# Optimization experiments

Measured on AMD Instinct MI355X. Metric: run time of the kernel, lower is better.

Reference implementation:

```python
import jax, jax.numpy as jnp
import numpy as np

OMEGA_ENC = 0.01   # Encoder.omega
OMEGA_K = 0.1      # KernelMLP.omega
N0, E0 = 4096, 16384     # level-0 graph
N1, E1 = 1024, 8192      # level-1 (pooled) graph
F_IN, H, LAT, DIM = 8, 64, 32, 3
F = H + DIM              # conv input features (x || pos)


def _glorot(key, shape):
    s = jnp.sqrt(2.0 / (shape[0] + shape[-1]))
    return (jax.random.normal(key, shape) * s).astype(jnp.float32)


def setup_inputs() -> dict:
    key = jax.random.key(0)
    ks = jax.random.split(key, 24)
    inp = {
        "x": jax.random.normal(ks[0], (N0, F_IN), jnp.float32),
        "pos": jax.random.normal(ks[1], (N0, DIM), jnp.float32),
        "edge_index": jax.random.randint(ks[2], (2, E0), 0, N0),
        "pool_edge_index1": jax.random.randint(ks[3], (2, E1), 0, N1),
        "pool_pos1": jax.random.normal(ks[4], (N1, DIM), jnp.float32),
        "pool_keep_idx0": jnp.sort(jax.random.randint(ks[5], (N1,), 0, N0)),
        "lin0_w": _glorot(ks[6], (F_IN, H)),
        "lin0_b": 0.01 * jax.random.normal(ks[7], (H,), jnp.float32),
        "lin1_w": _glorot(ks[8], (H, LAT)),
        "lin1_b": 0.01 * jax.random.normal(ks[9], (LAT,), jnp.float32),
    }
    k = 10
    for i in range(2):
        inp[f"conv{i}_k_w0"] = _glorot(ks[k], (DIM + 1, H))
        inp[f"conv{i}_k_b0"] = 0.01 * jax.random.normal(ks[k + 1], (H,), jnp.float32)
        inp[f"conv{i}_k_w1"] = _glorot(ks[k + 2], (H, H))
        inp[f"conv{i}_k_b1"] = 0.01 * jax.random.normal(ks[k + 3], (H,), jnp.float32)
        inp[f"conv{i}_k_w2"] = _glorot(ks[k + 4], (H, F))
        inp[f"conv{i}_k_b2"] = 0.01 * jax.random.normal(ks[k + 5], (F,), jnp.float32)
        inp[f"conv{i}_bias"] = jnp.zeros((H,), jnp.float32)  # zeros() init in torch
        k += 6
    return inp


def _with_self_loops(ei, n):
    # add_remaining_self_loops: input edges are assumed self-loop-free
    loops = jnp.arange(n, dtype=ei.dtype)
    return jnp.concatenate([ei, jnp.stack([loops, loops])], axis=1)


def _kernel_conv(xf, ei, pos, n, w0, b0, w1, b1, w2, b2, bias):
    src, dst = ei[0], ei[1]
    rel = pos[dst] - pos[src]                               # [E,3]
    zero = jnp.all(rel == 0.0, axis=1)                      # self loops -> rho=0, nan phi in torch
    rel_s = jnp.where(zero[:, None], 1.0, rel)              # safe values (avoid nan grads)
    rho = jnp.sqrt(jnp.sum(rel_s * rel_s, axis=1))
    theta = jnp.arctan2(rel_s[:, 1], rel_s[:, 0])
    phi = jnp.arcsin(jnp.clip(rel_s[:, 2] / rho, -1.0, 1.0))
    # torch sets theta/phi to 0 where phi is nan (rho==0); rho itself is 0 there
    rho = jnp.where(zero, 0.0, rho)
    theta = jnp.where(zero, 0.0, theta)
    phi = jnp.where(zero, 0.0, phi)
    feats = jnp.stack([rho, theta / jnp.pi, phi / jnp.pi], axis=1)   # [E,3]
    # KernelMLP lin0 on (feats || channel_id), evaluated for all out channels at once
    base = feats @ w0[:DIM] + b0                            # [E,H]
    ch = jnp.arange(H, dtype=xf.dtype)                      # out_channels == H
    h0 = jnp.sin(OMEGA_K * (base[None] + ch[:, None, None] * w0[DIM][None, None]))  # [C,E,H]
    h1 = jnp.sin(OMEGA_K * (jnp.einsum('ceh,hk->cek', h0, w1) + b1))                # [C,E,H]
    x_j = xf[src]                                           # [E,F]
    # msg[e,c] = (lin2(h1[c,e]) * x_j[e]).sum(); lin2 folded into the contraction
    msg = jnp.einsum('ceh,hf,ef->ec', h1, w2, x_j) + (x_j @ b2)[:, None]            # [E,C]
    return jax.ops.segment_sum(msg, dst, num_segments=n) + bias


def reference(x, edge_index, pos, pool_edge_index1, pool_pos1, pool_keep_idx0,
              lin0_w, lin0_b, lin1_w, lin1_b,
              conv0_k_w0, conv0_k_b0, conv0_k_w1, conv0_k_b1, conv0_k_w2, conv0_k_b2, conv0_bias,
              conv1_k_w0, conv1_k_b0, conv1_k_w1, conv1_k_b1, conv1_k_w2, conv1_k_b2, conv1_bias):
    n0 = x.shape[0]
    h = jnp.sin(OMEGA_ENC * (x @ lin0_w + lin0_b))
    ei0 = _with_self_loops(edge_index, n0)
    h = jnp.sin(OMEGA_ENC * _kernel_conv(jnp.concatenate([h, pos], 1), ei0, pos, n0,
                                         conv0_k_w0, conv0_k_b0, conv0_k_w1, conv0_k_b1,
                                         conv0_k_w2, conv0_k_b2, conv0_bias))
    # max_pool_neighbor_x: per-node max over neighbors incl. self (self loops in ei0)
    h = jax.ops.segment_max(h[ei0[0]], ei0[1], num_segments=n0)[pool_keep_idx0]
    n1 = pool_pos1.shape[0]
    ei1 = _with_self_loops(pool_edge_index1, n1)
    h = jnp.sin(OMEGA_ENC * _kernel_conv(jnp.concatenate([h, pool_pos1], 1), ei1, pool_pos1, n1,
                                         conv1_k_w0, conv1_k_b0, conv1_k_w1, conv1_k_b1,
                                         conv1_k_w2, conv1_k_b2, conv1_bias))
    return jnp.sin(OMEGA_ENC * (h @ lin1_w + lin1_b))   # [N1, LAT]
```

## Files before the change

kernel.cpp:

```cpp
#include <hip/hip_runtime.h>
#include <hip/hip_fp16.h>

#define N0C 4096
#define E0C 16384
#define N1C 1024
#define E1C 8192
#define HC 64
#define FINC 8
#define LATC 32
#define FC 67
#define E0T (E0C + N0C)
#define E1T (E1C + N1C)

typedef float f32x4 __attribute__((ext_vector_type(4)));
typedef _Float16 f16x8 __attribute__((ext_vector_type(8)));

__global__ void k_misc(const float* __restrict__ c0w0, const float* __restrict__ c1w0,
                       const float* __restrict__ c0w1, const float* __restrict__ c1w1,
                       const float* __restrict__ c0w2, const float* __restrict__ c1w2,
                       const int* __restrict__ ei0, const int* __restrict__ ei1,
                       _Float16* __restrict__ bC0, _Float16* __restrict__ bS0,
                       _Float16* __restrict__ bC1, _Float16* __restrict__ bS1,
                       _Float16* __restrict__ w1f0, _Float16* __restrict__ w1f1,
                       float* __restrict__ w2t0, float* __restrict__ w2t1,
                       int* __restrict__ cnt) {
  int id = blockIdx.x * blockDim.x + threadIdx.x;
  if (id < 8192) {
    int lvl = id >> 12, r = id & 4095;
    int fi = r >> 9, lane = (r >> 3) & 63, j = r & 7;
    int nt = fi & 3, ks = fi >> 2;
    int c = nt * 16 + (lane & 15);
    int h = ks * 32 + (lane >> 4) * 8 + j;
    const float* w = lvl ? c1w0 : c0w0;
    float s, cv;
    sincosf(0.1f * (float)c * w[3 * HC + h], &s, &cv);
    (lvl ? bC1 : bC0)[r] = (_Float16)cv;
    (lvl ? bS1 : bS0)[r] = (_Float16)s;
  } else if (id < 16384) {
    int r0 = id - 8192;
    int lvl = r0 >> 12, r = r0 & 4095;
    int fi = r >> 9, lane = (r >> 3) & 63, j = r & 7;
    int ms = fi & 3, ks = fi >> 2;
    int h = ks * 32 + (lane >> 4) * 8 + j;
    int kout = ms * 16 + (lane & 15);
    const float* w = lvl ? c1w1 : c0w1;
    (lvl ? w1f1 : w1f0)[r] = (_Float16)w[h * HC + kout];
  } else if (id < 24960) {
    int r = id - 16384;
    int lvl = r >= FC * HC;
    r -= lvl * FC * HC;
    int f = r >> 6, k = r & 63;
    (lvl ? w2t1 : w2t0)[r] = (lvl ? c1w2 : c0w2)[k * FC + f];
  } else if (id < 54656) {
    int r = id - 24960;
    if (r < E0T) {
      int dst = (r < E0C) ? ei0[E0C + r] : (r - E0C);
      atomicAdd(cnt + dst, 1);
    } else {
      int e = r - E0T;
      int dst = (e < E1C) ? ei1[E1C + e] : (e - E1C);
      atomicAdd(cnt + N0C + dst, 1);
    }
  }
}

__global__ void k_scan(const int* __restrict__ cnt, int* __restrict__ rp0,
                       int* __restrict__ rp1) {
  __shared__ int s[1024];
  const int b = blockIdx.x;
  const int n = b ? N1C : N0C;
  const int* c = cnt + (b ? N0C : 0);
  int* rp = b ? rp1 : rp0;
  const int tid = threadIdx.x;
  const int per = n >> 10;
  int loc[4];
  int sum = 0;
  for (int j = 0; j < per; ++j) { loc[j] = c[tid * per + j]; sum += loc[j]; }
  s[tid] = sum;
  __syncthreads();
  for (int off = 1; off < 1024; off <<= 1) {
    int v = s[tid] + ((tid >= off) ? s[tid - off] : 0);
    __syncthreads();
    s[tid] = v;
    __syncthreads();
  }
  int base = tid ? s[tid - 1] : 0;
  for (int j = 0; j < per; ++j) { rp[tid * per + j] = base; base += loc[j]; }
  if (tid == 1023) rp[n] = s[1023];
}

__global__ void k_scatter(const int* __restrict__ ei0, const int* __restrict__ ei1,
                          const int* __restrict__ rp0, const int* __restrict__ rp1,
                          int* __restrict__ fill, int* __restrict__ eidx0,
                          int* __restrict__ eidx1) {
  int id = blockIdx.x * blockDim.x + threadIdx.x;
  if (id < E0T) {
    int dst = (id < E0C) ? ei0[E0C + id] : (id - E0C);
    eidx0[rp0[dst] + atomicAdd(fill + dst, 1)] = id;
  } else if (id < E0T + E1T) {
    int e = id - E0T;
    int dst = (e < E1C) ? ei1[E1C + e] : (e - E1C);
    eidx1[rp1[dst] + atomicAdd(fill + N0C + dst, 1)] = e;
  }
}

__global__ void k_node0(const float* __restrict__ x, const float* __restrict__ l0w,
                        const float* __restrict__ l0b, const float* __restrict__ posp,
                        const float* __restrict__ w2t, const float* __restrict__ b2,
                        float* __restrict__ tN, float* __restrict__ dN) {
  __shared__ float xr[4][64];
  const int wave = threadIdx.x >> 6, lane = threadIdx.x & 63;
  const int n = blockIdx.x * 4 + wave;
  float a = l0b[lane];
#pragma unroll
  for (int f = 0; f < FINC; ++f) a = fmaf(x[n * FINC + f], l0w[f * HC + lane], a);
  xr[wave][lane] = sinf(0.01f * a);
  __syncthreads();
  const float px = posp[n * 3], py = posp[n * 3 + 1], pz = posp[n * 3 + 2];
  float tl = 0.f, ds = 0.f;
#pragma unroll 8
  for (int f = 0; f < HC; ++f) {
    float xv = xr[wave][f];
    tl = fmaf(xv, w2t[f * HC + lane], tl);
    ds = fmaf(xv, b2[f], ds);
  }
  tl = fmaf(px, w2t[64 * HC + lane], fmaf(py, w2t[65 * HC + lane], fmaf(pz, w2t[66 * HC + lane], tl)));
  ds = fmaf(px, b2[64], fmaf(py, b2[65], fmaf(pz, b2[66], ds)));
  tN[n * HC + lane] = tl;
  if (lane == 0) dN[n] = ds;
}

__global__ __launch_bounds__(256, 2) void k_conv(
    const int* __restrict__ ei, int E, int eTot,
    const float* __restrict__ posp,
    const float* __restrict__ tN, const float* __restrict__ dN,
    const float* __restrict__ kw0, const float* __restrict__ kb0,
    const _Float16* __restrict__ bC, const _Float16* __restrict__ bS,
    const _Float16* __restrict__ w1f, const float* __restrict__ b1,
    float* __restrict__ msg) {
  __shared__ _Float16 scS[4][64], scC[4][64];
  const int tid = threadIdx.x;
  const int wave = tid >> 6, lane = tid & 63;
  const int q = lane >> 4;

  f16x8 w1r[8], cbr[8], sbr[8];
#pragma unroll
  for (int f = 0; f < 8; ++f) {
    w1r[f] = *(const f16x8*)(w1f + ((f << 6) + lane) * 8);
    cbr[f] = *(const f16x8*)(bC + ((f << 6) + lane) * 8);
    sbr[f] = *(const f16x8*)(bS + ((f << 6) + lane) * 8);
  }
  const float kb0v = kb0[lane];
  const float kw0x = kw0[lane], kw0y = kw0[HC + lane], kw0z = kw0[2 * HC + lane];

  const int nW = gridDim.x * 4;
  for (int e = blockIdx.x * 4 + wave; e < eTot; e += nW) {
    int s, d2;
    if (e < E) { s = ei[e]; d2 = ei[E + e]; } else { s = e - E; d2 = s; }
    const float px = posp[s * 3], py = posp[s * 3 + 1], pz = posp[s * 3 + 2];
    const float rx = posp[d2 * 3] - px;
    const float ry = posp[d2 * 3 + 1] - py;
    const float rz = posp[d2 * 3 + 2] - pz;
    float f0 = 0.f, f1 = 0.f, f2 = 0.f;
    if (!(rx == 0.f && ry == 0.f && rz == 0.f)) {
      const float PI_F = 3.14159265358979323846f;
      float rho = sqrtf(rx * rx + ry * ry + rz * rz);
      float th = atan2f(ry, rx);
      float ratio = fminf(1.f, fmaxf(-1.f, rz / rho));
      float ph = asinf(ratio);
      f0 = rho; f1 = th / PI_F; f2 = ph / PI_F;
    }
    float base = fmaf(f0, kw0x, fmaf(f1, kw0y, fmaf(f2, kw0z, kb0v)));
    float sv, cv;
    sincosf(0.1f * base, &sv, &cv);
    scS[wave][lane] = (_Float16)sv;
    scC[wave][lane] = (_Float16)cv;
    __builtin_amdgcn_wave_barrier();

    f16x8 bf[2][4];
#pragma unroll
    for (int ks = 0; ks < 2; ++ks) {
      f16x8 sv8 = *(const f16x8*)&scS[wave][ks * 32 + q * 8];
      f16x8 cv8 = *(const f16x8*)&scC[wave][ks * 32 + q * 8];
#pragma unroll
      for (int nt = 0; nt < 4; ++nt)
        bf[ks][nt] = sv8 * cbr[ks * 4 + nt] + cv8 * sbr[ks * 4 + nt];
    }

    f32x4 acc[4][4];
    const f32x4 zero = {0.f, 0.f, 0.f, 0.f};
#pragma unroll
    for (int ms = 0; ms < 4; ++ms)
#pragma unroll
      for (int nt = 0; nt < 4; ++nt) acc[ms][nt] = zero;
#pragma unroll
    for (int ks = 0; ks < 2; ++ks)
#pragma unroll
      for (int ms = 0; ms < 4; ++ms)
#pragma unroll
        for (int nt = 0; nt < 4; ++nt)
          acc[ms][nt] = __builtin_amdgcn_mfma_f32_16x16x32_f16(
              w1r[ks * 4 + ms], bf[ks][nt], acc[ms][nt], 0, 0, 0);

    const float dv = dN[s];
    float snt0 = 0.f, snt1 = 0.f, snt2 = 0.f, snt3 = 0.f;
#pragma unroll
    for (int ms = 0; ms < 4; ++ms) {
      f32x4 tv = *(const f32x4*)(tN + (size_t)s * HC + ms * 16 + q * 4);
      f32x4 bv = *(const f32x4*)(b1 + ms * 16 + q * 4);
#pragma unroll
      for (int r = 0; r < 4; ++r) {
        float bb = 0.1f * bv[r], tt = tv[r];
        snt0 = fmaf(__sinf(fmaf(0.1f, acc[ms][0][r], bb)), tt, snt0);
        snt1 = fmaf(__sinf(fmaf(0.1f, acc[ms][1][r], bb)), tt, snt1);
        snt2 = fmaf(__sinf(fmaf(0.1f, acc[ms][2][r], bb)), tt, snt2);
        snt3 = fmaf(__sinf(fmaf(0.1f, acc[ms][3][r], bb)), tt, snt3);
      }
    }
    snt0 += __shfl_xor(snt0, 16, 64); snt0 += __shfl_xor(snt0, 32, 64);
    snt1 += __shfl_xor(snt1, 16, 64); snt1 += __shfl_xor(snt1, 32, 64);
    snt2 += __shfl_xor(snt2, 16, 64); snt2 += __shfl_xor(snt2, 32, 64);
    snt3 += __shfl_xor(snt3, 16, 64); snt3 += __shfl_xor(snt3, 32, 64);
    float val = (q == 0) ? snt0 : (q == 1) ? snt1 : (q == 2) ? snt2 : snt3;
    msg[(size_t)e * HC + lane] = val + dv;
  }
}

__global__ void k_reduce(const float* __restrict__ msg, const int* __restrict__ eidx,
                         const int* __restrict__ rp, const float* __restrict__ bias,
                         float* __restrict__ outp, int n) {
  int wave = threadIdx.x >> 6, lane = threadIdx.x & 63;
  int node = blockIdx.x * 4 + wave;
  if (node >= n) return;
  int j0 = rp[node], j1 = rp[node + 1];
  float s = 0.f;
  for (int j = j0; j < j1; ++j) s += msg[(size_t)eidx[j] * HC + lane];
  outp[node * HC + lane] = sinf(0.01f * (s + bias[lane]));
}

__global__ void k_pool1(const float* __restrict__ hc0, const int* __restrict__ eidx,
                        const int* __restrict__ rp, const int* __restrict__ ei,
                        const int* __restrict__ keep, const float* __restrict__ ppos,
                        const float* __restrict__ w2t, const float* __restrict__ b2,
                        float* __restrict__ tN, float* __restrict__ dN) {
  __shared__ float xr[4][64];
  const int wave = threadIdx.x >> 6, lane = threadIdx.x & 63;
  const int i = blockIdx.x * 4 + wave;
  int n = keep[i];
  int j0 = rp[n], j1 = rp[n + 1];
  float m = -INFINITY;
  for (int j = j0; j < j1; ++j) {
    int e = eidx[j];
    int src = (e < E0C) ? ei[e] : (e - E0C);
    m = fmaxf(m, hc0[(size_t)src * HC + lane]);
  }
  xr[wave][lane] = m;
  __syncthreads();
  const float px = ppos[i * 3], py = ppos[i * 3 + 1], pz = ppos[i * 3 + 2];
  float tl = 0.f, ds = 0.f;
#pragma unroll 8
  for (int f = 0; f < HC; ++f) {
    float xv = xr[wave][f];
    tl = fmaf(xv, w2t[f * HC + lane], tl);
    ds = fmaf(xv, b2[f], ds);
  }
  tl = fmaf(px, w2t[64 * HC + lane], fmaf(py, w2t[65 * HC + lane], fmaf(pz, w2t[66 * HC + lane], tl)));
  ds = fmaf(px, b2[64], fmaf(py, b2[65], fmaf(pz, b2[66], ds)));
  tN[i * HC + lane] = tl;
  if (lane == 0) dN[i] = ds;
}

__global__ void k_reduce1f(const float* __restrict__ msg, const int* __restrict__ eidx,
                           const int* __restrict__ rp, const float* __restrict__ bias,
                           const float* __restrict__ l1w, const float* __restrict__ l1b,
                           float* __restrict__ outp) {
  __shared__ float hr[4][64];
  const int wave = threadIdx.x >> 6, lane = threadIdx.x & 63;
  const int node = blockIdx.x * 4 + wave;
  int j0 = rp[node], j1 = rp[node + 1];
  float s = 0.f;
  for (int j = j0; j < j1; ++j) s += msg[(size_t)eidx[j] * HC + lane];
  hr[wave][lane] = sinf(0.01f * (s + bias[lane]));
  __syncthreads();
  if (lane < 32) {
    float o = l1b[lane];
#pragma unroll 8
    for (int c = 0; c < HC; ++c) o = fmaf(hr[wave][c], l1w[c * LATC + lane], o);
    outp[node * LATC + lane] = sinf(0.01f * o);
  }
}

extern "C" void kernel_launch(void* const* d_in, const int* in_sizes, int n_in,
                              void* d_out, int out_size, void* d_ws, size_t ws_size,
                              hipStream_t stream) {
  (void)in_sizes; (void)n_in; (void)out_size; (void)ws_size;
  const float* x    = (const float*)d_in[0];
  const float* pos  = (const float*)d_in[1];
  const int*   ei   = (const int*)d_in[2];
  const int*   pei  = (const int*)d_in[3];
  const float* ppos = (const float*)d_in[4];
  const int*   keep = (const int*)d_in[5];
  const float* l0w  = (const float*)d_in[6];
  const float* l0b  = (const float*)d_in[7];
  const float* l1w  = (const float*)d_in[8];
  const float* l1b  = (const float*)d_in[9];
  const float* c0w0 = (const float*)d_in[10];
  const float* c0b0 = (const float*)d_in[11];
  const float* c0w1 = (const float*)d_in[12];
  const float* c0b1 = (const float*)d_in[13];
  const float* c0w2 = (const float*)d_in[14];
  const float* c0b2 = (const float*)d_in[15];
  const float* c0bias = (const float*)d_in[16];
  const float* c1w0 = (const float*)d_in[17];
  const float* c1b0 = (const float*)d_in[18];
  const float* c1w1 = (const float*)d_in[19];
  const float* c1b1 = (const float*)d_in[20];
  const float* c1w2 = (const float*)d_in[21];
  const float* c1b2 = (const float*)d_in[22];
  const float* c1bias = (const float*)d_in[23];
  float* outp = (float*)d_out;

  char* p = (char*)d_ws;
  auto carve = [&](size_t bytes) -> char* {
    char* r = p;
    p += (bytes + 255) & ~(size_t)255;
    return r;
  };
  float* hc0  = (float*)carve((size_t)N0C * HC * 4);
  float* tN0  = (float*)carve((size_t)N0C * HC * 4);
  float* dN0  = (float*)carve((size_t)N0C * 4);
  float* tN1  = (float*)carve((size_t)N1C * HC * 4);
  float* dN1  = (float*)carve((size_t)N1C * 4);
  _Float16* bC0  = (_Float16*)carve(4096 * 2);
  _Float16* bS0  = (_Float16*)carve(4096 * 2);
  _Float16* bC1  = (_Float16*)carve(4096 * 2);
  _Float16* bS1  = (_Float16*)carve(4096 * 2);
  _Float16* w1f0 = (_Float16*)carve(4096 * 2);
  _Float16* w1f1 = (_Float16*)carve(4096 * 2);
  float* w2t0 = (float*)carve((size_t)FC * HC * 4);
  float* w2t1 = (float*)carve((size_t)FC * HC * 4);
  int* cnt  = (int*)carve((size_t)(N0C + N1C) * 4);
  int* fill = (int*)carve((size_t)(N0C + N1C) * 4);
  int* rp0 = (int*)carve((size_t)(N0C + 1) * 4);
  int* rp1 = (int*)carve((size_t)(N1C + 1) * 4);
  int* eidx0 = (int*)carve((size_t)E0T * 4);
  int* eidx1 = (int*)carve((size_t)E1T * 4);
  float* msg = (float*)carve((size_t)E0T * HC * 4);

  hipMemsetAsync(cnt, 0, (size_t)(N0C + N1C) * 4 * 2, stream);

  k_misc<<<214, 256, 0, stream>>>(c0w0, c1w0, c0w1, c1w1, c0w2, c1w2, ei, pei,
                                  bC0, bS0, bC1, bS1, w1f0, w1f1, w2t0, w2t1, cnt);
  k_scan<<<2, 1024, 0, stream>>>(cnt, rp0, rp1);
  k_scatter<<<(E0T + E1T + 255) / 256, 256, 0, stream>>>(ei, pei, rp0, rp1, fill,
                                                         eidx0, eidx1);
  k_node0<<<N0C / 4, 256, 0, stream>>>(x, l0w, l0b, pos, w2t0, c0b2, tN0, dN0);

  k_conv<<<512, 256, 0, stream>>>(ei, E0C, E0T, pos, tN0, dN0, c0w0, c0b0,
                                  bC0, bS0, w1f0, c0b1, msg);
  k_reduce<<<N0C / 4, 256, 0, stream>>>(msg, eidx0, rp0, c0bias, hc0, N0C);
  k_pool1<<<N1C / 4, 256, 0, stream>>>(hc0, eidx0, rp0, ei, keep, ppos, w2t1, c1b2,
                                       tN1, dN1);

  k_conv<<<512, 256, 0, stream>>>(pei, E1C, E1T, ppos, tN1, dN1, c1w0, c1b0,
                                  bC1, bS1, w1f1, c1b1, msg);
  k_reduce1f<<<N1C / 4, 256, 0, stream>>>(msg, eidx1, rp1, c1bias, l1w, l1b, outp);
}
```

Baseline: 194.4 us.

## Fuse edge conv with per-node reduction via CSR and merge prep kernels

```diff
diff --git a/kernel.cpp b/kernel.cpp
--- a/kernel.cpp
+++ b/kernel.cpp
@@ -15,51 +15,74 @@
 typedef float f32x4 __attribute__((ext_vector_type(4)));
 typedef _Float16 f16x8 __attribute__((ext_vector_type(8)));
 
-__global__ void k_misc(const float* __restrict__ c0w0, const float* __restrict__ c1w0,
-                       const float* __restrict__ c0w1, const float* __restrict__ c1w1,
-                       const float* __restrict__ c0w2, const float* __restrict__ c1w2,
-                       const int* __restrict__ ei0, const int* __restrict__ ei1,
-                       _Float16* __restrict__ bC0, _Float16* __restrict__ bS0,
-                       _Float16* __restrict__ bC1, _Float16* __restrict__ bS1,
-                       _Float16* __restrict__ w1f0, _Float16* __restrict__ w1f1,
-                       float* __restrict__ w2t0, float* __restrict__ w2t1,
-                       int* __restrict__ cnt) {
-  int id = blockIdx.x * blockDim.x + threadIdx.x;
-  if (id < 8192) {
-    int lvl = id >> 12, r = id & 4095;
-    int fi = r >> 9, lane = (r >> 3) & 63, j = r & 7;
-    int nt = fi & 3, ks = fi >> 2;
-    int c = nt * 16 + (lane & 15);
-    int h = ks * 32 + (lane >> 4) * 8 + j;
-    const float* w = lvl ? c1w0 : c0w0;
-    float s, cv;
-    sincosf(0.1f * (float)c * w[3 * HC + h], &s, &cv);
-    (lvl ? bC1 : bC0)[r] = (_Float16)cv;
-    (lvl ? bS1 : bS0)[r] = (_Float16)s;
-  } else if (id < 16384) {
-    int r0 = id - 8192;
-    int lvl = r0 >> 12, r = r0 & 4095;
-    int fi = r >> 9, lane = (r >> 3) & 63, j = r & 7;
-    int ms = fi & 3, ks = fi >> 2;
-    int h = ks * 32 + (lane >> 4) * 8 + j;
-    int kout = ms * 16 + (lane & 15);
-    const float* w = lvl ? c1w1 : c0w1;
-    (lvl ? w1f1 : w1f0)[r] = (_Float16)w[h * HC + kout];
-  } else if (id < 24960) {
-    int r = id - 16384;
-    int lvl = r >= FC * HC;
-    r -= lvl * FC * HC;
-    int f = r >> 6, k = r & 63;
-    (lvl ? w2t1 : w2t0)[r] = (lvl ? c1w2 : c0w2)[k * FC + f];
-  } else if (id < 54656) {
-    int r = id - 24960;
-    if (r < E0T) {
-      int dst = (r < E0C) ? ei0[E0C + r] : (r - E0C);
-      atomicAdd(cnt + dst, 1);
-    } else {
-      int e = r - E0T;
-      int dst = (e < E1C) ? ei1[E1C + e] : (e - E1C);
-      atomicAdd(cnt + N0C + dst, 1);
+__global__ __launch_bounds__(256) void k_prep(
+    const float* __restrict__ x, const float* __restrict__ l0w,
+    const float* __restrict__ l0b, const float* __restrict__ posp,
+    const float* __restrict__ c0w2, const float* __restrict__ c0b2,
+    const float* __restrict__ c0w0, const float* __restrict__ c1w0,
+    const float* __restrict__ c0w1, const float* __restrict__ c1w1,
+    const int* __restrict__ ei0, const int* __restrict__ ei1,
+    _Float16* __restrict__ bC0, _Float16* __restrict__ bS0,
+    _Float16* __restrict__ bC1, _Float16* __restrict__ bS1,
+    _Float16* __restrict__ w1f0, _Float16* __restrict__ w1f1,
+    int* __restrict__ cnt, float* __restrict__ tN, float* __restrict__ dN) {
+  if (blockIdx.x < 1024) {
+    __shared__ float w2s[64][69];
+    __shared__ float xr[4][64];
+    const int tid = threadIdx.x;
+    const int wave = __builtin_amdgcn_readfirstlane(tid >> 6), lane = tid & 63;
+    for (int idx = tid; idx < HC * FC; idx += 256)
+      w2s[idx / FC][idx % FC] = c0w2[idx];
+    const int n = blockIdx.x * 4 + wave;
+    float a = l0b[lane];
+#pragma unroll
+    for (int f = 0; f < FINC; ++f) a = fmaf(x[n * FINC + f], l0w[f * HC + lane], a);
+    xr[wave][lane] = sinf(0.01f * a);
+    __syncthreads();
+    const float px = posp[n * 3], py = posp[n * 3 + 1], pz = posp[n * 3 + 2];
+    float tl = 0.f, ds = 0.f;
+#pragma unroll 8
+    for (int f = 0; f < HC; ++f) {
+      float xv = xr[wave][f];
+      tl = fmaf(xv, w2s[lane][f], tl);
+      ds = fmaf(xv, c0b2[f], ds);
+    }
+    tl = fmaf(px, w2s[lane][64], fmaf(py, w2s[lane][65], fmaf(pz, w2s[lane][66], tl)));
+    ds = fmaf(px, c0b2[64], fmaf(py, c0b2[65], fmaf(pz, c0b2[66], ds)));
+    tN[n * HC + lane] = tl;
+    if (lane == 0) dN[n] = ds;
+  } else {
+    int id = (blockIdx.x - 1024) * 256 + threadIdx.x;
+    if (id < 8192) {
+      int lvl = id >> 12, r = id & 4095;
+      int fi = r >> 9, lane = (r >> 3) & 63, j = r & 7;
+      int nt = fi & 3, ks = fi >> 2;
+      int c = nt * 16 + (lane & 15);
+      int h = ks * 32 + (lane >> 4) * 8 + j;
+      const float* w = lvl ? c1w0 : c0w0;
+      float s, cv;
+      sincosf(0.1f * (float)c * w[3 * HC + h], &s, &cv);
+      (lvl ? bC1 : bC0)[r] = (_Float16)cv;
+      (lvl ? bS1 : bS0)[r] = (_Float16)s;
+    } else if (id < 16384) {
+      int r0 = id - 8192;
+      int lvl = r0 >> 12, r = r0 & 4095;
+      int fi = r >> 9, lane = (r >> 3) & 63, j = r & 7;
+      int ms = fi & 3, ks = fi >> 2;
+      int h = ks * 32 + (lane >> 4) * 8 + j;
+      int kout = ms * 16 + (lane & 15);
+      const float* w = lvl ? c1w1 : c0w1;
+      (lvl ? w1f1 : w1f0)[r] = (_Float16)w[h * HC + kout];
+    } else if (id < 16384 + E0T + E1T) {
+      int r = id - 16384;
+      if (r < E0T) {
+        int dst = (r < E0C) ? ei0[E0C + r] : (r - E0C);
+        atomicAdd(cnt + dst, 1);
+      } else {
+        int e = r - E0T;
+        int dst = (e < E1C) ? ei1[E1C + e] : (e - E1C);
+        atomicAdd(cnt + N0C + dst, 1);
+      }
     }
   }
 }
@@ -104,59 +127,44 @@
   }
 }
 
-__global__ void k_node0(const float* __restrict__ x, const float* __restrict__ l0w,
-                        const float* __restrict__ l0b, const float* __restrict__ posp,
-                        const float* __restrict__ w2t, const float* __restrict__ b2,
-                        float* __restrict__ tN, float* __restrict__ dN) {
-  __shared__ float xr[4][64];
-  const int wave = threadIdx.x >> 6, lane = threadIdx.x & 63;
-  const int n = blockIdx.x * 4 + wave;
-  float a = l0b[lane];
-#pragma unroll
-  for (int f = 0; f < FINC; ++f) a = fmaf(x[n * FINC + f], l0w[f * HC + lane], a);
-  xr[wave][lane] = sinf(0.01f * a);
-  __syncthreads();
-  const float px = posp[n * 3], py = posp[n * 3 + 1], pz = posp[n * 3 + 2];
-  float tl = 0.f, ds = 0.f;
-#pragma unroll 8
-  for (int f = 0; f < HC; ++f) {
-    float xv = xr[wave][f];
-    tl = fmaf(xv, w2t[f * HC + lane], tl);
-    ds = fmaf(xv, b2[f], ds);
-  }
-  tl = fmaf(px, w2t[64 * HC + lane], fmaf(py, w2t[65 * HC + lane], fmaf(pz, w2t[66 * HC + lane], tl)));
-  ds = fmaf(px, b2[64], fmaf(py, b2[65], fmaf(pz, b2[66], ds)));
-  tN[n * HC + lane] = tl;
-  if (lane == 0) dN[n] = ds;
-}
-
-__global__ __launch_bounds__(256, 2) void k_conv(
-    const int* __restrict__ ei, int E, int eTot,
-    const float* __restrict__ posp,
+__global__ __launch_bounds__(256, 3) void k_conv0(
+    const int* __restrict__ ei, const int* __restrict__ rp,
+    const int* __restrict__ eidx, const float* __restrict__ posp,
     const float* __restrict__ tN, const float* __restrict__ dN,
     const float* __restrict__ kw0, const float* __restrict__ kb0,
     const _Float16* __restrict__ bC, const _Float16* __restrict__ bS,
     const _Float16* __restrict__ w1f, const float* __restrict__ b1,
-    float* __restrict__ msg) {
-  __shared__ _Float16 scS[4][64], scC[4][64];
+    const float* __restrict__ bias, float* __restrict__ hc) {
+  __shared__ __attribute__((aligned(16))) _Float16 bCs[4096], bSs[4096];
+  __shared__ __attribute__((aligned(16))) _Float16 scS[4][64], scC[4][64];
   const int tid = threadIdx.x;
-  const int wave = tid >> 6, lane = tid & 63;
+  const int wave = __builtin_amdgcn_readfirstlane(tid >> 6), lane = tid & 63;
   const int q = lane >> 4;
-
-  f16x8 w1r[8], cbr[8], sbr[8];
-#pragma unroll
-  for (int f = 0; f < 8; ++f) {
-    w1r[f] = *(const f16x8*)(w1f + ((f << 6) + lane) * 8);
-    cbr[f] = *(const f16x8*)(bC + ((f << 6) + lane) * 8);
-    sbr[f] = *(const f16x8*)(bS + ((f << 6) + lane) * 8);
+  for (int idx = tid; idx < 512; idx += 256) {
+    ((f16x8*)bCs)[idx] = ((const f16x8*)bC)[idx];
+    ((f16x8*)bSs)[idx] = ((const f16x8*)bS)[idx];
+  }
+  f16x8 w1r[8];
+#pragma unroll
+  for (int f = 0; f < 8; ++f) w1r[f] = *(const f16x8*)(w1f + ((f << 6) + lane) * 8);
+  f32x4 bb[4];
+#pragma unroll
+  for (int ms = 0; ms < 4; ++ms) {
+    f32x4 t = *(const f32x4*)(b1 + ms * 16 + q * 4);
+    bb[ms] = t * 0.1f;
   }
   const float kb0v = kb0[lane];
   const float kw0x = kw0[lane], kw0y = kw0[HC + lane], kw0z = kw0[2 * HC + lane];
-
-  const int nW = gridDim.x * 4;
-  for (int e = blockIdx.x * 4 + wave; e < eTot; e += nW) {
+  const float biasl = bias[lane];
+  __syncthreads();
+
+  const int n = blockIdx.x * 4 + wave;
+  const int j0 = rp[n], j1 = rp[n + 1];
+  float snt0 = 0.f, snt1 = 0.f, snt2 = 0.f, snt3 = 0.f, dsum = 0.f;
+  for (int j = j0; j < j1; ++j) {
+    const int e = eidx[j];
     int s, d2;
-    if (e < E) { s = ei[e]; d2 = ei[E + e]; } else { s = e - E; d2 = s; }
+    if (e < E0C) { s = ei[e]; d2 = ei[E0C + e]; } else { s = e - E0C; d2 = s; }
     const float px = posp[s * 3], py = posp[s * 3 + 1], pz = posp[s * 3 + 2];
     const float rx = posp[d2 * 3] - px;
     const float ry = posp[d2 * 3 + 1] - py;
@@ -177,74 +185,65 @@
     scC[wave][lane] = (_Float16)cv;
     __builtin_amdgcn_wave_barrier();
 
-    f16x8 bf[2][4];
+    f32x4 acc[4][4];
+    const f32x4 zero = {0.f, 0.f, 0.f, 0.f};
+#pragma unroll
+    for (int ms = 0; ms < 4; ++ms)
+#pragma unroll
+      for (int nt = 0; nt < 4; ++nt) acc[ms][nt] = zero;
 #pragma unroll
     for (int ks = 0; ks < 2; ++ks) {
       f16x8 sv8 = *(const f16x8*)&scS[wave][ks * 32 + q * 8];
       f16x8 cv8 = *(const f16x8*)&scC[wave][ks * 32 + q * 8];
-#pragma unroll
-      for (int nt = 0; nt < 4; ++nt)
-        bf[ks][nt] = sv8 * cbr[ks * 4 + nt] + cv8 * sbr[ks * 4 + nt];
-    }
-
-    f32x4 acc[4][4];
-    const f32x4 zero = {0.f, 0.f, 0.f, 0.f};
-#pragma unroll
-    for (int ms = 0; ms < 4; ++ms)
-#pragma unroll
-      for (int nt = 0; nt < 4; ++nt) acc[ms][nt] = zero;
-#pragma unroll
-    for (int ks = 0; ks < 2; ++ks)
+      f16x8 bf[4];
+#pragma unroll
+      for (int nt = 0; nt < 4; ++nt) {
+        f16x8 cb = *(const f16x8*)&bCs[((ks * 4 + nt) * 64 + lane) * 8];
+        f16x8 sb = *(const f16x8*)&bSs[((ks * 4 + nt) * 64 + lane) * 8];
+        bf[nt] = sv8 * cb + cv8 * sb;
+      }
 #pragma unroll
       for (int ms = 0; ms < 4; ++ms)
 #pragma unroll
         for (int nt = 0; nt < 4; ++nt)
           acc[ms][nt] = __builtin_amdgcn_mfma_f32_16x16x32_f16(
-              w1r[ks * 4 + ms], bf[ks][nt], acc[ms][nt], 0, 0, 0);
-
-    const float dv = dN[s];
-    float snt0 = 0.f, snt1 = 0.f, snt2 = 0.f, snt3 = 0.f;
+              w1r[ks * 4 + ms], bf[nt], acc[ms][nt], 0, 0, 0);
+    }
+
+    const float* tr = tN + (size_t)s * HC;
+    dsum += dN[s];
 #pragma unroll
     for (int ms = 0; ms < 4; ++ms) {
-      f32x4 tv = *(const f32x4*)(tN + (size_t)s * HC + ms * 16 + q * 4);
-      f32x4 bv = *(const f32x4*)(b1 + ms * 16 + q * 4);
+      f32x4 tv = *(const f32x4*)(tr + ms * 16 + q * 4);
 #pragma unroll
       for (int r = 0; r < 4; ++r) {
-        float bb = 0.1f * bv[r], tt = tv[r];
-        snt0 = fmaf(__sinf(fmaf(0.1f, acc[ms][0][r], bb)), tt, snt0);
-        snt1 = fmaf(__sinf(fmaf(0.1f, acc[ms][1][r], bb)), tt, snt1);
-        snt2 = fmaf(__sinf(fmaf(0.1f, acc[ms][2][r], bb)), tt, snt2);
-        snt3 = fmaf(__sinf(fmaf(0.1f, acc[ms][3][r], bb)), tt, snt3);
+        float tt = tv[r];
+        snt0 = fmaf(__sinf(fmaf(0.1f, acc[ms][0][r], bb[ms][r])), tt, snt0);
+        snt1 = fmaf(__sinf(fmaf(0.1f, acc[ms][1][r], bb[ms][r])), tt, snt1);
+        snt2 = fmaf(__sinf(fmaf(0.1f, acc[ms][2][r], bb[ms][r])), tt, snt2);
+        snt3 = fmaf(__sinf(fmaf(0.1f, acc[ms][3][r], bb[ms][r])), tt, snt3);
       }
     }
-    snt0 += __shfl_xor(snt0, 16, 64); snt0 += __shfl_xor(snt0, 32, 64);
-    snt1 += __shfl_xor(snt1, 16, 64); snt1 += __shfl_xor(snt1, 32, 64);
-    snt2 += __shfl_xor(snt2, 16, 64); snt2 += __shfl_xor(snt2, 32, 64);
-    snt3 += __shfl_xor(snt3, 16, 64); snt3 += __shfl_xor(snt3, 32, 64);
-    float val = (q == 0) ? snt0 : (q == 1) ? snt1 : (q == 2) ? snt2 : snt3;
-    msg[(size_t)e * HC + lane] = val + dv;
-  }
-}
-
-__global__ void k_reduce(const float* __restrict__ msg, const int* __restrict__ eidx,
-                         const int* __restrict__ rp, const float* __restrict__ bias,
-                         float* __restrict__ outp, int n) {
-  int wave = threadIdx.x >> 6, lane = threadIdx.x & 63;
-  int node = blockIdx.x * 4 + wave;
-  if (node >= n) return;
-  int j0 = rp[node], j1 = rp[node + 1];
-  float s = 0.f;
-  for (int j = j0; j < j1; ++j) s += msg[(size_t)eidx[j] * HC + lane];
-  outp[node * HC + lane] = sinf(0.01f * (s + bias[lane]));
+  }
+  snt0 += __shfl_xor(snt0, 16, 64); snt0 += __shfl_xor(snt0, 32, 64);
+  snt1 += __shfl_xor(snt1, 16, 64); snt1 += __shfl_xor(snt1, 32, 64);
+  snt2 += __shfl_xor(snt2, 16, 64); snt2 += __shfl_xor(snt2, 32, 64);
+  snt3 += __shfl_xor(snt3, 16, 64); snt3 += __shfl_xor(snt3, 32, 64);
+  float val = (q == 0) ? snt0 : (q == 1) ? snt1 : (q == 2) ? snt2 : snt3;
+  hc[(size_t)n * HC + lane] = sinf(0.01f * (val + dsum + biasl));
 }
 
 __global__ void k_pool1(const float* __restrict__ hc0, const int* __restrict__ eidx,
                         const int* __restrict__ rp, const int* __restrict__ ei,
                         const int* __restrict__ keep, const float* __restrict__ ppos,
-                        const float* __restrict__ w2t, const float* __restrict__ b2,
+                        const float* __restrict__ c1w2, const float* __restrict__ c1b2,
                         float* __restrict__ tN, float* __restrict__ dN) {
+  __shared__ float w2s[64][69];
   __shared__ float xr[4][64];
-  const int wave = threadIdx.x >> 6, lane = threadIdx.x & 63;
+  const int tid = threadIdx.x;
+  const int wave = __builtin_amdgcn_readfirstlane(tid >> 6), lane = tid & 63;
+  for (int idx = tid; idx < HC * FC; idx += 256)
+    w2s[idx / FC][idx % FC] = c1w2[idx];
   const int i = blockIdx.x * 4 + wave;
   int n = keep[i];
   int j0 = rp[n], j1 = rp[n + 1];
@@ -261,31 +260,133 @@
 #pragma unroll 8
   for (int f = 0; f < HC; ++f) {
     float xv = xr[wave][f];
-    tl = fmaf(xv, w2t[f * HC + lane], tl);
-    ds = fmaf(xv, b2[f], ds);
-  }
-  tl = fmaf(px, w2t[64 * HC + lane], fmaf(py, w2t[65 * HC + lane], fmaf(pz, w2t[66 * HC + lane], tl)));
-  ds = fmaf(px, b2[64], fmaf(py, b2[65], fmaf(pz, b2[66], ds)));
+    tl = fmaf(xv, w2s[lane][f], tl);
+    ds = fmaf(xv, c1b2[f], ds);
+  }
+  tl = fmaf(px, w2s[lane][64], fmaf(py, w2s[lane][65], fmaf(pz, w2s[lane][66], tl)));
+  ds = fmaf(px, c1b2[64], fmaf(py, c1b2[65], fmaf(pz, c1b2[66], ds)));
   tN[i * HC + lane] = tl;
   if (lane == 0) dN[i] = ds;
 }
 
-__global__ void k_reduce1f(const float* __restrict__ msg, const int* __restrict__ eidx,
-                           const int* __restrict__ rp, const float* __restrict__ bias,
-                           const float* __restrict__ l1w, const float* __restrict__ l1b,
-                           float* __restrict__ outp) {
-  __shared__ float hr[4][64];
-  const int wave = threadIdx.x >> 6, lane = threadIdx.x & 63;
-  const int node = blockIdx.x * 4 + wave;
-  int j0 = rp[node], j1 = rp[node + 1];
-  float s = 0.f;
-  for (int j = j0; j < j1; ++j) s += msg[(size_t)eidx[j] * HC + lane];
-  hr[wave][lane] = sinf(0.01f * (s + bias[lane]));
-  __syncthreads();
-  if (lane < 32) {
+__global__ __launch_bounds__(256, 3) void k_conv1(
+    const int* __restrict__ ei, const int* __restrict__ rp,
+    const int* __restrict__ eidx, const float* __restrict__ posp,
+    const float* __restrict__ tN, const float* __restrict__ dN,
+    const float* __restrict__ kw0, const float* __restrict__ kb0,
+    const _Float16* __restrict__ bC, const _Float16* __restrict__ bS,
+    const _Float16* __restrict__ w1f, const float* __restrict__ b1,
+    const float* __restrict__ bias, const float* __restrict__ l1w,
+    const float* __restrict__ l1b, float* __restrict__ outp) {
+  __shared__ __attribute__((aligned(16))) _Float16 bCs[4096], bSs[4096];
+  __shared__ __attribute__((aligned(16))) _Float16 scS[4][64], scC[4][64];
+  __shared__ float part[4][64];
+  __shared__ float hr[2][64];
+  const int tid = threadIdx.x;
+  const int wave = __builtin_amdgcn_readfirstlane(tid >> 6), lane = tid & 63;
+  const int q = lane >> 4;
+  for (int idx = tid; idx < 512; idx += 256) {
+    ((f16x8*)bCs)[idx] = ((const f16x8*)bC)[idx];
+    ((f16x8*)bSs)[idx] = ((const f16x8*)bS)[idx];
+  }
+  f16x8 w1r[8];
+#pragma unroll
+  for (int f = 0; f < 8; ++f) w1r[f] = *(const f16x8*)(w1f + ((f << 6) + lane) * 8);
+  f32x4 bb[4];
+#pragma unroll
+  for (int ms = 0; ms < 4; ++ms) {
+    f32x4 t = *(const f32x4*)(b1 + ms * 16 + q * 4);
+    bb[ms] = t * 0.1f;
+  }
+  const float kb0v = kb0[lane];
+  const float kw0x = kw0[lane], kw0y = kw0[HC + lane], kw0z = kw0[2 * HC + lane];
+  __syncthreads();
+
+  const int node = blockIdx.x * 2 + (wave >> 1);
+  const int seg = wave & 1;
+  const int j0 = rp[node], j1 = rp[node + 1];
+  float snt0 = 0.f, snt1 = 0.f, snt2 = 0.f, snt3 = 0.f, dsum = 0.f;
+  for (int j = j0 + seg; j < j1; j += 2) {
+    const int e = eidx[j];
+    int s, d2;
+    if (e < E1C) { s = ei[e]; d2 = ei[E1C + e]; } else { s = e - E1C; d2 = s; }
+    const float px = posp[s * 3], py = posp[s * 3 + 1], pz = posp[s * 3 + 2];
+    const float rx = posp[d2 * 3] - px;
+    const float ry = posp[d2 * 3 + 1] - py;
+    const float rz = posp[d2 * 3 + 2] - pz;
+    float f0 = 0.f, f1 = 0.f, f2 = 0.f;
+    if (!(rx == 0.f && ry == 0.f && rz == 0.f)) {
+      const float PI_F = 3.14159265358979323846f;
+      float rho = sqrtf(rx * rx + ry * ry + rz * rz);
+      float th = atan2f(ry, rx);
+      float ratio = fminf(1.f, fmaxf(-1.f, rz / rho));
+      float ph = asinf(ratio);
+      f0 = rho; f1 = th / PI_F; f2 = ph / PI_F;
+    }
+    float base = fmaf(f0, kw0x, fmaf(f1, kw0y, fmaf(f2, kw0z, kb0v)));
+    float sv, cv;
+    sincosf(0.1f * base, &sv, &cv);
+    scS[wave][lane] = (_Float16)sv;
+    scC[wave][lane] = (_Float16)cv;
+    __builtin_amdgcn_wave_barrier();
+
+    f32x4 acc[4][4];
+    const f32x4 zero = {0.f, 0.f, 0.f, 0.f};
+#pragma unroll
+    for (int ms = 0; ms < 4; ++ms)
+#pragma unroll
+      for (int nt = 0; nt < 4; ++nt) acc[ms][nt] = zero;
+#pragma unroll
+    for (int ks = 0; ks < 2; ++ks) {
+      f16x8 sv8 = *(const f16x8*)&scS[wave][ks * 32 + q * 8];
+      f16x8 cv8 = *(const f16x8*)&scC[wave][ks * 32 + q * 8];
+      f16x8 bf[4];
+#pragma unroll
+      for (int nt = 0; nt < 4; ++nt) {
+        f16x8 cb = *(const f16x8*)&bCs[((ks * 4 + nt) * 64 + lane) * 8];
+        f16x8 sb = *(const f16x8*)&bSs[((ks * 4 + nt) * 64 + lane) * 8];
+        bf[nt] = sv8 * cb + cv8 * sb;
+      }
+#pragma unroll
+      for (int ms = 0; ms < 4; ++ms)
+#pragma unroll
+        for (int nt = 0; nt < 4; ++nt)
+          acc[ms][nt] = __builtin_amdgcn_mfma_f32_16x16x32_f16(
+              w1r[ks * 4 + ms], bf[nt], acc[ms][nt], 0, 0, 0);
+    }
+
+    const float* tr = tN + (size_t)s * HC;
+    dsum += dN[s];
+#pragma unroll
+    for (int ms = 0; ms < 4; ++ms) {
+      f32x4 tv = *(const f32x4*)(tr + ms * 16 + q * 4);
+#pragma unroll
+      for (int r = 0; r < 4; ++r) {
+        float tt = tv[r];
+        snt0 = fmaf(__sinf(fmaf(0.1f, acc[ms][0][r], bb[ms][r])), tt, snt0);
+        snt1 = fmaf(__sinf(fmaf(0.1f, acc[ms][1][r], bb[ms][r])), tt, snt1);
+        snt2 = fmaf(__sinf(fmaf(0.1f, acc[ms][2][r], bb[ms][r])), tt, snt2);
+        snt3 = fmaf(__sinf(fmaf(0.1f, acc[ms][3][r], bb[ms][r])), tt, snt3);
+      }
+    }
+  }
+  snt0 += __shfl_xor(snt0, 16, 64); snt0 += __shfl_xor(snt0, 32, 64);
+  snt1 += __shfl_xor(snt1, 16, 64); snt1 += __shfl_xor(snt1, 32, 64);
+  snt2 += __shfl_xor(snt2, 16, 64); snt2 += __shfl_xor(snt2, 32, 64);
+  snt3 += __shfl_xor(snt3, 16, 64); snt3 += __shfl_xor(snt3, 32, 64);
+  float val = (q == 0) ? snt0 : (q == 1) ? snt1 : (q == 2) ? snt2 : snt3;
+  part[wave][lane] = val + dsum;
+  __syncthreads();
+  if (seg == 0) {
+    float tot = part[wave][lane] + part[wave + 1][lane];
+    hr[wave >> 1][lane] = sinf(0.01f * (tot + bias[lane]));
+  }
+  __syncthreads();
+  if (seg == 1 && lane < LATC) {
+    const float* h = hr[wave >> 1];
     float o = l1b[lane];
 #pragma unroll 8
-    for (int c = 0; c < HC; ++c) o = fmaf(hr[wave][c], l1w[c * LATC + lane], o);
+    for (int c = 0; c < HC; ++c) o = fmaf(h[c], l1w[c * LATC + lane], o);
     outp[node * LATC + lane] = sinf(0.01f * o);
   }
 }
@@ -337,32 +438,28 @@
   _Float16* bS1  = (_Float16*)carve(4096 * 2);
   _Float16* w1f0 = (_Float16*)carve(4096 * 2);
   _Float16* w1f1 = (_Float16*)carve(4096 * 2);
-  float* w2t0 = (float*)carve((size_t)FC * HC * 4);
-  float* w2t1 = (float*)carve((size_t)FC * HC * 4);
   int* cnt  = (int*)carve((size_t)(N0C + N1C) * 4);
   int* fill = (int*)carve((size_t)(N0C + N1C) * 4);
   int* rp0 = (int*)carve((size_t)(N0C + 1) * 4);
   int* rp1 = (int*)carve((size_t)(N1C + 1) * 4);
   int* eidx0 = (int*)carve((size_t)E0T * 4);
   int* eidx1 = (int*)carve((size_t)E1T * 4);
-  float* msg = (float*)carve((size_t)E0T * HC * 4);
 
   hipMemsetAsync(cnt, 0, (size_t)(N0C + N1C) * 4 * 2, stream);
 
-  k_misc<<<214, 256, 0, stream>>>(c0w0, c1w0, c0w1, c1w1, c0w2, c1w2, ei, pei,
-                                  bC0, bS0, bC1, bS1, w1f0, w1f1, w2t0, w2t1, cnt);
+  k_prep<<<1024 + 180, 256, 0, stream>>>(x, l0w, l0b, pos, c0w2, c0b2,
+                                         c0w0, c1w0, c0w1, c1w1, ei, pei,
+                                         bC0, bS0, bC1, bS1, w1f0, w1f1,
+                                         cnt, tN0, dN0);
   k_scan<<<2, 1024, 0, stream>>>(cnt, rp0, rp1);
   k_scatter<<<(E0T + E1T + 255) / 256, 256, 0, stream>>>(ei, pei, rp0, rp1, fill,
                                                          eidx0, eidx1);
-  k_node0<<<N0C / 4, 256, 0, stream>>>(x, l0w, l0b, pos, w2t0, c0b2, tN0, dN0);
-
-  k_conv<<<512, 256, 0, stream>>>(ei, E0C, E0T, pos, tN0, dN0, c0w0, c0b0,
-                                  bC0, bS0, w1f0, c0b1, msg);
-  k_reduce<<<N0C / 4, 256, 0, stream>>>(msg, eidx0, rp0, c0bias, hc0, N0C);
-  k_pool1<<<N1C / 4, 256, 0, stream>>>(hc0, eidx0, rp0, ei, keep, ppos, w2t1, c1b2,
-                                       tN1, dN1);
-
-  k_conv<<<512, 256, 0, stream>>>(pei, E1C, E1T, ppos, tN1, dN1, c1w0, c1b0,
-                                  bC1, bS1, w1f1, c1b1, msg);
-  k_reduce1f<<<N1C / 4, 256, 0, stream>>>(msg, eidx1, rp1, c1bias, l1w, l1b, outp);
-}
+  k_conv0<<<N0C / 4, 256, 0, stream>>>(ei, rp0, eidx0, pos, tN0, dN0,
+                                       c0w0, c0b0, bC0, bS0, w1f0, c0b1,
+                                       c0bias, hc0);
+  k_pool1<<<N1C / 4, 256, 0, stream>>>(hc0, eidx0, rp0, ei, keep, ppos,
+                                       c1w2, c1b2, tN1, dN1);
+  k_conv1<<<N1C / 2, 256, 0, stream>>>(pei, rp1, eidx1, ppos, tN1, dN1,
+                                       c1w0, c1b0, bC1, bS1, w1f1, c1b1,
+                                       c1bias, l1w, l1b, outp);
+}
```

New measurement: 198.0 us. No clear change (+1.8%).
